# Optimization experiments

Hardware: AMD Instinct MI355X
Metric: run time of the kernel (lower is better)

The kernel has to match this reference:

```python
import jax, jax.numpy as jnp
import numpy as np

TOPK = 8
NGRAM = 3
D = 256
VOCAB = 5000


def build_scores_mask(seq_len, topk, ngram):
    # Replicates PREFIX.__init__ mask construction then the [:S*k,:S*k] slice
    # and the ~(...) inversion: True = disallowed (masked out).
    # Chunk-level: query chunk i may attend key chunks j in [i-1, i+ngram-2], j != i.
    L = seq_len
    allowed = np.zeros((L, L), dtype=bool)
    for i in range(L):
        for j in range(max(0, i - 1), min(L, i + ngram - 1)):
            if j != i:
                allowed[i, j] = True
    tok = np.kron(allowed, np.ones((topk, topk), dtype=bool))  # (L*k, L*k)
    return jnp.asarray(~tok)


def setup_inputs() -> dict:
    key = jax.random.key(0)
    k1, k2, k3, k4 = jax.random.split(key, 4)
    bsz, seq_len = 64, 128
    na_pred = jax.random.normal(k1, (bsz, seq_len, VOCAB), dtype=jnp.float32)
    emb_table = jax.random.normal(k2, (VOCAB, D), dtype=jnp.float32) * 0.02
    Wq = jax.random.normal(k3, (D, D), dtype=jnp.float32) / np.sqrt(D)
    Wk = jax.random.normal(k4, (D, D), dtype=jnp.float32) / np.sqrt(D)
    bq = jnp.zeros((D,), dtype=jnp.float32)
    bk = jnp.zeros((D,), dtype=jnp.float32)
    return {"bsz": bsz, "seq_len": seq_len, "na_pred": na_pred,
            "emb_table": emb_table, "Wq": Wq, "bq": bq, "Wk": Wk, "bk": bk}


def reference(bsz, seq_len, na_pred, emb_table, Wq, bq, Wk, bk):
    k, g = TOPK, NGRAM
    # top-k prefix candidates and their renormalized probabilities
    probs = jax.nn.softmax(na_pred, axis=-1)                 # (b, S, V)
    na_prefix_prob, na_prefix = jax.lax.top_k(probs, k)     # (b, S, k)
    na_prefix_prob = jax.nn.softmax(na_prefix_prob, axis=-1)
    # gather prefix embeddings (espnet-style sqrt(d) scale)
    prefix_emb = emb_table[na_prefix] * jnp.asarray(np.sqrt(D), na_pred.dtype)  # (b,S,k,D)
    prefix_emb = prefix_emb.reshape(bsz, seq_len * k, D)
    # ScoreAttention over gathered prefixes with ngram block mask
    q = prefix_emb @ Wq + bq
    kk = prefix_emb @ Wk + bk
    scores = jnp.einsum('bqd,bkd->bqk', q, kk) / jnp.asarray(np.sqrt(D), q.dtype)
    mask = build_scores_mask(seq_len, k, g)                  # (S*k, S*k) True=masked
    scores = jnp.where(mask[None], jnp.asarray(-1e9, scores.dtype), scores)
    attn = jax.nn.softmax(scores, axis=-1)                   # (b, S*k, S*k)
    # per-candidate score = incoming attention mass
    na_score = attn.sum(axis=1).reshape(bsz, seq_len, k)
    # elementwise mul with candidate prob, L1 normalize (F.normalize p=1 eps=1e-12)
    prefix_score = na_score * na_prefix_prob
    l1 = jnp.maximum(jnp.sum(jnp.abs(prefix_score), axis=-1, keepdims=True), 1e-12)
    prefix_score = prefix_score / l1                         # (b, S, k)
    # weighted reduce over candidates
    prefix_emb4 = prefix_emb.reshape(bsz, seq_len, k, D)
    scored_prefix = jnp.sum(prefix_emb4 * prefix_score[..., None], axis=2)  # (b, S, D)
    return scored_prefix, prefix_score, na_prefix
```

## Files before the change

kernel.cpp:

```cpp
#include <hip/hip_runtime.h>
#include <math.h>

#define TOPK 8
#define D    256
#define VOCAB 5000
#define BSZ  64
#define SEQ  128
#define ROWS (BSZ*SEQ)
#define NF4  (VOCAB/4)

#define OFF_IDX    0
#define OFF_NPP    262144
#define OFF_M      524288
#define OFF_W      787456
#define OFF_P      790528
#define OFF_NPART  5910528
#define OFF_KBV    6434816
#define OFF_WMAX   6455296
#define OFF_WSUM   6586368
#define OFF_WCNT   6717440
#define OFF_WCAND  6848512

#define OUT_SCORED 0
#define OUT_PS     2097152
#define OUT_IDX    2162688

typedef unsigned long long u64;
typedef unsigned int u32;

__device__ __forceinline__ float wave_fsum(float v) {
    #pragma unroll
    for (int st = 1; st < 64; st <<= 1) v += __shfl_xor(v, st, 64);
    return v;
}
__device__ __forceinline__ u64 wave_umax(u64 v) {
    #pragma unroll
    for (int st = 1; st < 64; st <<= 1) {
        const u64 o = __shfl_xor(v, st, 64);
        v = (o > v) ? o : v;
    }
    return v;
}
__device__ __forceinline__ u64 pack_key(float x, int idx) {
    u32 bu = __float_as_uint(x);
    u32 key = bu ^ ((u32)((int)bu >> 31) | 0x80000000u);
    return ((u64)key << 32) | (u64)(0xFFFFFFFFu ^ (u32)idx);
}

__global__ __launch_bounds__(256) void topk_pass1(
    const float* __restrict__ na_pred,
    float* __restrict__ wmaxA, float* __restrict__ wsumA,
    int*   __restrict__ wcntA, u64* __restrict__ wcandA)
{
    const int row  = blockIdx.x;
    const int wid  = threadIdx.x >> 6;
    const int lane = threadIdx.x & 63;
    const int wgid = row * 4 + wid;

    const float4* src = (const float4*)(na_pred + (long long)row * VOCAB) + wid * 320;
    const int nf4 = (wid == 3) ? 290 : 320;

    float4 rr[5];
    #pragma unroll
    for (int j = 0; j < 5; ++j) {
        const int i4 = lane + 64*j;
        rr[j] = (i4 < nf4) ? src[i4]
              : make_float4(-INFINITY, -INFINITY, -INFINITY, -INFINITY);
    }

    float lm = -INFINITY;
    #pragma unroll
    for (int j = 0; j < 5; ++j)
        lm = fmaxf(lm, fmaxf(fmaxf(rr[j].x, rr[j].y), fmaxf(rr[j].z, rr[j].w)));

    int c = 0;
    #pragma unroll
    for (int j = 0; j < 64; ++j) {
        const float o = __shfl(lm, j, 64);
        c += (o > lm || (o == lm && j < lane)) ? 1 : 0;
    }
    const u64 b0 = __ballot(c == 0);
    const u64 b7 = __ballot(c == 7);
    const float wmax = __shfl(lm, (int)(__ffsll(b0) - 1), 64);
    const float thr  = __shfl(lm, (int)(__ffsll(b7) - 1), 64);

    float se = 0.f;
    #pragma unroll
    for (int j = 0; j < 5; ++j) {
        se += __expf(rr[j].x - wmax) + __expf(rr[j].y - wmax)
            + __expf(rr[j].z - wmax) + __expf(rr[j].w - wmax);
    }
    const float S = wave_fsum(se);

    int ct = 0;
    #pragma unroll
    for (int j = 0; j < 5; ++j)
        ct += (rr[j].x >= thr) + (rr[j].y >= thr) + (rr[j].z >= thr) + (rr[j].w >= thr);

    int v = ct;
    #pragma unroll
    for (int d = 1; d < 64; d <<= 1) {
        const int o = __shfl_up(v, d, 64);
        if (lane >= d) v += o;
    }
    const int total = __shfl(v, 63, 64);

    u64* myc = wcandA + (long long)wgid * 64;
    int run = v - ct;
    #pragma unroll
    for (int j = 0; j < 5; ++j) {
        const int e0 = wid*1280 + 4*(lane + 64*j);
        const float vv[4] = {rr[j].x, rr[j].y, rr[j].z, rr[j].w};
        #pragma unroll
        for (int cc = 0; cc < 4; ++cc) {
            if (vv[cc] >= thr) {
                if (run < 64) myc[run] = pack_key(vv[cc], e0 + cc);
                ++run;
            }
        }
    }
    if (lane == 63) {
        wmaxA[wgid] = wmax;
        wsumA[wgid] = S;
        wcntA[wgid] = total;
    }
}

__global__ __launch_bounds__(256) void topk_pass2(
    const float* __restrict__ na_pred,
    const float* __restrict__ wmaxA, const float* __restrict__ wsumA,
    const int*   __restrict__ wcntA, const u64* __restrict__ wcandA,
    int*  __restrict__ out_idx,
    float* __restrict__ out_npp,
    float* __restrict__ out_idx_f)
{
    __shared__ u64   ck[256];
    __shared__ float wm4[4], ws4[4];
    __shared__ int   wc4[4];
    __shared__ u64   res_s[8];
    __shared__ u64   ured[4];

    const int row = blockIdx.x;
    const int tid = threadIdx.x;
    const int lane = tid & 63;
    const int wid  = tid >> 6;

    if (tid < 4) {
        wm4[tid] = wmaxA[row*4 + tid];
        ws4[tid] = wsumA[row*4 + tid];
        wc4[tid] = wcntA[row*4 + tid];
    }
    if (tid < 8) res_s[tid] = 0xFFFFFFFFULL;
    __syncthreads();

    const int c0 = wc4[0], c1 = wc4[1], c2 = wc4[2], c3 = wc4[3];
    const bool ovf = (c0 > 64) || (c1 > 64) || (c2 > 64) || (c3 > 64);
    const float rowmax = fmaxf(fmaxf(wm4[0], wm4[1]), fmaxf(wm4[2], wm4[3]));
    const float S = ws4[0]*__expf(wm4[0]-rowmax) + ws4[1]*__expf(wm4[1]-rowmax)
                  + ws4[2]*__expf(wm4[2]-rowmax) + ws4[3]*__expf(wm4[3]-rowmax);

    const int cw = min(wc4[wid], 64);
    u64 mine = 0ULL;
    if (lane < cw) mine = wcandA[(long long)(row*4 + wid)*64 + lane];
    ck[tid] = mine;
    __syncthreads();

    if (!ovf) {
        const int n0 = min(c0,64), n1 = min(c1,64), n2 = min(c2,64), n3 = min(c3,64);
        int c = 0;
        for (int j = 0;       j < n0;       ++j) c += (ck[j]       > mine) ? 1 : 0;
        for (int j = 0;       j < n1;       ++j) c += (ck[64+j]    > mine) ? 1 : 0;
        for (int j = 0;       j < n2;       ++j) c += (ck[128+j]   > mine) ? 1 : 0;
        for (int j = 0;       j < n3;       ++j) c += (ck[192+j]   > mine) ? 1 : 0;
        if (mine != 0ULL && c < 8) res_s[c] = mine;
    } else {
        const float4* srcr = (const float4*)(na_pred + (long long)row * VOCAB);
        const int i0 = tid, i1 = tid+256, i2 = tid+512, i3 = tid+768, i4 = tid+1024;
        const float4 r0 = srcr[i0];
        const float4 r1 = srcr[i1];
        const float4 r2 = srcr[i2];
        const float4 r3 = srcr[i3];
        const float4 r4 = (i4 < NF4) ? srcr[i4]
                        : make_float4(-INFINITY, -INFINITY, -INFINITY, -INFINITY);
        u64 last = ~0ULL;
        #pragma unroll 1
        for (int r = 0; r < 8; ++r) {
            u64 best = 0ULL;
#define CAND(val, eidx) do { const u64 k_ = pack_key((val), (eidx)); \
    if (k_ < last && k_ > best) best = k_; } while (0)
            CAND(r0.x, 4*i0+0); CAND(r0.y, 4*i0+1); CAND(r0.z, 4*i0+2); CAND(r0.w, 4*i0+3);
            CAND(r1.x, 4*i1+0); CAND(r1.y, 4*i1+1); CAND(r1.z, 4*i1+2); CAND(r1.w, 4*i1+3);
            CAND(r2.x, 4*i2+0); CAND(r2.y, 4*i2+1); CAND(r2.z, 4*i2+2); CAND(r2.w, 4*i2+3);
            CAND(r3.x, 4*i3+0); CAND(r3.y, 4*i3+1); CAND(r3.z, 4*i3+2); CAND(r3.w, 4*i3+3);
            CAND(r4.x, 4*i4+0); CAND(r4.y, 4*i4+1); CAND(r4.z, 4*i4+2); CAND(r4.w, 4*i4+3);
#undef CAND
            best = wave_umax(best);
            if (lane == 0) ured[wid] = best;
            __syncthreads();
            u64 b = ured[0];
            #pragma unroll
            for (int wq = 1; wq < 4; ++wq) b = (ured[wq] > b) ? ured[wq] : b;
            if (tid == 0) res_s[r] = b;
            last = b;
            __syncthreads();
        }
    }
    __syncthreads();

    if (wid == 0 && lane < 8) {
        const u64 res = res_s[lane];
        const u32 key = (u32)(res >> 32);
        const int ixv = (int)(0xFFFFFFFFu ^ (u32)(res & 0xFFFFFFFFu));
        const u32 bu  = key ^ ((key & 0x80000000u) ? 0x80000000u : 0xFFFFFFFFu);
        const float p = __expf(__uint_as_float(bu) - rowmax) / S;
        float pm = p;
        #pragma unroll
        for (int st = 1; st < 8; st <<= 1) pm = fmaxf(pm, __shfl_xor(pm, st, 64));
        const float q = __expf(p - pm);
        float s2 = q;
        #pragma unroll
        for (int st = 1; st < 8; st <<= 1) s2 += __shfl_xor(s2, st, 64);
        const long long ob = (long long)row * TOPK + lane;
        out_idx[ob]   = ixv;
        out_npp[ob]   = q / s2;
        out_idx_f[ob] = (float)ixv;
    }
}

__global__ __launch_bounds__(256) void mw_kernel(
    const float* __restrict__ Wq, const float* __restrict__ Wk,
    const float* __restrict__ bq,
    float* __restrict__ M, float* __restrict__ w)
{
    __shared__ float qrow[D];
    const int j = threadIdx.x;
    if (blockIdx.x < D) {
        const int a = blockIdx.x;
        qrow[j] = Wq[a*D + j];
        __syncthreads();
        float acc = 0.f;
        #pragma unroll 4
        for (int d4 = 0; d4 < 64; ++d4) {
            const float4 wk = *(const float4*)&Wk[j*D + 4*d4];
            const float4 q4 = *(const float4*)&qrow[4*d4];
            acc += wk.x*q4.x + wk.y*q4.y + wk.z*q4.z + wk.w*q4.w;
        }
        M[a*D + j] = acc;
    } else {
        float aw = 0.f;
        #pragma unroll 4
        for (int d4 = 0; d4 < 64; ++d4) {
            const float4 wk = *(const float4*)&Wk[j*D + 4*d4];
            const float4 b4 = *(const float4*)&bq[4*d4];
            aw += wk.x*b4.x + wk.y*b4.y + wk.z*b4.z + wk.w*b4.w;
        }
        w[j] = aw;
    }
}

__global__ __launch_bounds__(256) void kbv_kernel(
    const float* __restrict__ E, const float* __restrict__ w,
    float* __restrict__ kbv)
{
    const int row  = blockIdx.x * 4 + (threadIdx.x >> 6);
    const int lane = threadIdx.x & 63;
    if (row >= VOCAB) return;
    const float4 e  = *(const float4*)&E[(long long)row*D + 4*lane];
    const float4 ww = *(const float4*)&w[4*lane];
    float p = e.x*ww.x + e.y*ww.y + e.z*ww.z + e.w*ww.w;
    #pragma unroll
    for (int st = 1; st < 64; st <<= 1) p += __shfl_xor(p, st, 64);
    if (lane == 0) kbv[row] = p;
}

__global__ __launch_bounds__(256) void p_kernel(
    const float* __restrict__ E, const float* __restrict__ M,
    float* __restrict__ P)
{
    __shared__ float seT[256][20];
    const int tid = threadIdx.x;
    const int r0  = blockIdx.x * 16;
    {
        const int r = tid >> 4, d4b = tid & 15;
        const bool ok = (r0 + r) < VOCAB;
        #pragma unroll
        for (int k = 0; k < 4; ++k) {
            const int d4 = d4b + 16*k;
            float4 v = make_float4(0.f, 0.f, 0.f, 0.f);
            if (ok) v = *(const float4*)&E[(long long)(r0+r)*D + 4*d4];
            seT[4*d4+0][r] = v.x; seT[4*d4+1][r] = v.y;
            seT[4*d4+2][r] = v.z; seT[4*d4+3][r] = v.w;
        }
    }
    __syncthreads();
    const int rg = tid >> 6, j4 = tid & 63;
    float acc[4][4];
    #pragma unroll
    for (int i = 0; i < 4; ++i)
        { acc[i][0]=0.f; acc[i][1]=0.f; acc[i][2]=0.f; acc[i][3]=0.f; }
    #pragma unroll 4
    for (int d = 0; d < 256; ++d) {
        const float4 m4 = *(const float4*)&M[d*D + 4*j4];
        const float4 s4 = *(const float4*)&seT[d][4*rg];
        const float ss[4] = {s4.x, s4.y, s4.z, s4.w};
        #pragma unroll
        for (int rr = 0; rr < 4; ++rr) {
            acc[rr][0] += ss[rr]*m4.x; acc[rr][1] += ss[rr]*m4.y;
            acc[rr][2] += ss[rr]*m4.z; acc[rr][3] += ss[rr]*m4.w;
        }
    }
    #pragma unroll
    for (int rr = 0; rr < 4; ++rr) {
        const int row = r0 + 4*rg + rr;
        if (row < VOCAB) {
            float4 o;
            o.x = acc[rr][0]; o.y = acc[rr][1]; o.z = acc[rr][2]; o.w = acc[rr][3];
            *(float4*)&P[(long long)row*D + 4*j4] = o;
        }
    }
}

__global__ __launch_bounds__(64) void attn_kernel(
    const float* __restrict__ P, const float* __restrict__ E,
    const int*  __restrict__ idx, const float* __restrict__ kbv,
    float* __restrict__ na_part )
{
    const int blk = blockIdx.x;
    const int b = blk >> 7, s = blk & 127;
    const int tid = threadIdx.x;

    __shared__ float Ps[8][260];
    __shared__ float Es[16][260];
    __shared__ int   qidx[8];
    __shared__ int   kidx[16];
    __shared__ float kb[16];
    __shared__ int   kchs[2];

    int kcl[2]; int nk = 0;
    if (s > 0)       kcl[nk++] = s - 1;
    if (s < SEQ - 1) kcl[nk++] = s + 1;
    const int nkeys = nk * 8;

    if (tid < 2 && tid < nk) kchs[tid] = kcl[tid];
    if (tid < 8) qidx[tid] = idx[blk*8 + tid];
    if (tid < 16) {
        if (tid < nkeys) {
            const int v = idx[(b*SEQ + kcl[tid >> 3])*8 + (tid & 7)];
            kidx[tid] = v;
            kb[tid]   = kbv[v];
        } else { kidx[tid] = 0; kb[tid] = 0.f; }
    }
    __syncthreads();

    #pragma unroll
    for (int r = 0; r < 8; ++r)
        *(float4*)&Ps[r][4*tid] = *(const float4*)&P[(long long)qidx[r]*D + 4*tid];
    for (int r = 0; r < 16; ++r)
        if (r < nkeys)
            *(float4*)&Es[r][4*tid] = *(const float4*)&E[(long long)kidx[r]*D + 4*tid];
    __syncthreads();

    const int qp = tid >> 4, ki = tid & 15;
    float acc0 = 0.f, acc1 = 0.f;
    const float* pr0 = Ps[qp];
    const float* pr1 = Ps[qp + 4];
    const float* er  = Es[ki];
    #pragma unroll 4
    for (int d4 = 0; d4 < 64; ++d4) {
        const float4 e  = *(const float4*)&er[4*d4];
        const float4 p0 = *(const float4*)&pr0[4*d4];
        const float4 p1 = *(const float4*)&pr1[4*d4];
        acc0 += p0.x*e.x + p0.y*e.y + p0.z*e.z + p0.w*e.w;
        acc1 += p1.x*e.x + p1.y*e.y + p1.z*e.z + p1.w*e.w;
    }
    const bool kvalid = ki < nkeys;
    const float s0 = kvalid ? (16.f*acc0 + kb[ki]) : -1e30f;
    const float s1 = kvalid ? (16.f*acc1 + kb[ki]) : -1e30f;

    float m0 = s0, m1 = s1;
    #pragma unroll
    for (int st = 1; st < 16; st <<= 1) {
        m0 = fmaxf(m0, __shfl_xor(m0, st, 64));
        m1 = fmaxf(m1, __shfl_xor(m1, st, 64));
    }
    float e0 = kvalid ? __expf(s0 - m0) : 0.f;
    float e1 = kvalid ? __expf(s1 - m1) : 0.f;
    float t0 = e0, t1 = e1;
    #pragma unroll
    for (int st = 1; st < 16; st <<= 1) {
        t0 += __shfl_xor(t0, st, 64);
        t1 += __shfl_xor(t1, st, 64);
    }
    const float a0 = e0 / t0, a1 = e1 / t1;

    float cs = a0 + a1;
    cs += __shfl_xor(cs, 16, 64);
    cs += __shfl_xor(cs, 32, 64);
    if (tid < 16 && kvalid) {
        const int kc   = kchs[tid >> 3];
        const int slot = (kc == s + 1) ? 0 : 1;
        na_part[((b*SEQ + kc)*2 + slot)*8 + (tid & 7)] = cs;
    }
}

__global__ __launch_bounds__(256) void finalize_kernel(
    const float* __restrict__ E, const int* __restrict__ idx,
    const float* __restrict__ npp, const float* __restrict__ na_part,
    float* __restrict__ out)
{
    const int blk = blockIdx.x;
    const int s   = blk & 127;
    const int tid = threadIdx.x;
    __shared__ float ps[8];
    __shared__ int   id8[8];

    if (tid < 8) {
        const long long t = (long long)blk*8 + tid;
        float ns = 0.f;
        if (s >= 1)       ns += na_part[((long long)blk*2 + 0)*8 + tid];
        if (s <= SEQ - 2) ns += na_part[((long long)blk*2 + 1)*8 + tid];
        ps[tid] = ns * npp[t];
        id8[tid] = idx[t];
    }
    __syncthreads();
    if (tid == 0) {
        float l1 = 0.f;
        #pragma unroll
        for (int r = 0; r < 8; ++r) l1 += fabsf(ps[r]);
        l1 = fmaxf(l1, 1e-12f);
        #pragma unroll
        for (int r = 0; r < 8; ++r) ps[r] /= l1;
    }
    __syncthreads();

    float acc = 0.f;
    #pragma unroll
    for (int r = 0; r < 8; ++r) acc += E[(long long)id8[r]*D + tid] * ps[r];
    out[OUT_SCORED + (long long)blk*D + tid] = acc * 16.f;
    if (tid < 8) out[OUT_PS + (long long)blk*8 + tid] = ps[tid];
}

extern "C" void kernel_launch(void* const* d_in, const int* in_sizes, int n_in,
                              void* d_out, int out_size, void* d_ws, size_t ws_size,
                              hipStream_t stream)
{
    const float* na_pred = (const float*)d_in[2];
    const float* emb     = (const float*)d_in[3];
    const float* Wq      = (const float*)d_in[4];
    const float* bq      = (const float*)d_in[5];
    const float* Wk      = (const float*)d_in[6];
    const float* bk      = (const float*)d_in[7];
    (void)bk;

    char* ws = (char*)d_ws;
    int*   ws_idx  = (int*)  (ws + OFF_IDX);
    float* ws_npp  = (float*)(ws + OFF_NPP);
    float* ws_M    = (float*)(ws + OFF_M);
    float* ws_w    = (float*)(ws + OFF_W);
    float* ws_P    = (float*)(ws + OFF_P);
    float* ws_np   = (float*)(ws + OFF_NPART);
    float* ws_kbv  = (float*)(ws + OFF_KBV);
    float* ws_wmax = (float*)(ws + OFF_WMAX);
    float* ws_wsum = (float*)(ws + OFF_WSUM);
    int*   ws_wcnt = (int*)  (ws + OFF_WCNT);
    u64*   ws_wcnd = (u64*)  (ws + OFF_WCAND);
    float* out     = (float*)d_out;

    topk_pass1<<<ROWS, 256, 0, stream>>>(na_pred, ws_wmax, ws_wsum, ws_wcnt, ws_wcnd);
    topk_pass2<<<ROWS, 256, 0, stream>>>(na_pred, ws_wmax, ws_wsum, ws_wcnt, ws_wcnd,
                                         ws_idx, ws_npp, out + OUT_IDX);
    mw_kernel<<<D + 1, 256, 0, stream>>>(Wq, Wk, bq, ws_M, ws_w);
    kbv_kernel<<<(VOCAB + 3)/4, 256, 0, stream>>>(emb, ws_w, ws_kbv);
    p_kernel<<<(VOCAB + 15)/16, 256, 0, stream>>>(emb, ws_M, ws_P);
    attn_kernel<<<ROWS, 64, 0, stream>>>(ws_P, emb, ws_idx, ws_kbv, ws_np);
    finalize_kernel<<<ROWS, 256, 0, stream>>>(emb, ws_idx, ws_npp, ws_np, out);
}
```

Before: 142.0 us.

## Fuse two-pass top-k into one kernel with 4 rows per block and prefetch

Merges the two top-k kernels into one, so per-wave candidates, maxima and sums stay in shared memory instead of round-tripping through global workspace. Each block now handles four rows and prefetches the next row's logits into registers while the current row is processed. The overflow fallback reuses the register-resident data instead of re-reading the row from global memory. This removes a launch and the workspace traffic, at the cost of fewer blocks (2048), more registers and serial per-row work within a block.

```diff
diff --git a/kernel.cpp b/kernel.cpp
--- a/kernel.cpp
+++ b/kernel.cpp
@@ -16,10 +16,6 @@
 #define OFF_P      790528
 #define OFF_NPART  5910528
 #define OFF_KBV    6434816
-#define OFF_WMAX   6455296
-#define OFF_WSUM   6586368
-#define OFF_WCNT   6717440
-#define OFF_WCAND  6848512
 
 #define OUT_SCORED 0
 #define OUT_PS     2097152
@@ -47,183 +43,156 @@
     return ((u64)key << 32) | (u64)(0xFFFFFFFFu ^ (u32)idx);
 }
 
-__global__ __launch_bounds__(256) void topk_pass1(
+__global__ __launch_bounds__(256) void topk_kernel(
     const float* __restrict__ na_pred,
-    float* __restrict__ wmaxA, float* __restrict__ wsumA,
-    int*   __restrict__ wcntA, u64* __restrict__ wcandA)
-{
-    const int row  = blockIdx.x;
-    const int wid  = threadIdx.x >> 6;
-    const int lane = threadIdx.x & 63;
-    const int wgid = row * 4 + wid;
-
-    const float4* src = (const float4*)(na_pred + (long long)row * VOCAB) + wid * 320;
-    const int nf4 = (wid == 3) ? 290 : 320;
-
-    float4 rr[5];
-    #pragma unroll
-    for (int j = 0; j < 5; ++j) {
-        const int i4 = lane + 64*j;
-        rr[j] = (i4 < nf4) ? src[i4]
-              : make_float4(-INFINITY, -INFINITY, -INFINITY, -INFINITY);
-    }
-
-    float lm = -INFINITY;
-    #pragma unroll
-    for (int j = 0; j < 5; ++j)
-        lm = fmaxf(lm, fmaxf(fmaxf(rr[j].x, rr[j].y), fmaxf(rr[j].z, rr[j].w)));
-
-    int c = 0;
-    #pragma unroll
-    for (int j = 0; j < 64; ++j) {
-        const float o = __shfl(lm, j, 64);
-        c += (o > lm || (o == lm && j < lane)) ? 1 : 0;
-    }
-    const u64 b0 = __ballot(c == 0);
-    const u64 b7 = __ballot(c == 7);
-    const float wmax = __shfl(lm, (int)(__ffsll(b0) - 1), 64);
-    const float thr  = __shfl(lm, (int)(__ffsll(b7) - 1), 64);
-
-    float se = 0.f;
-    #pragma unroll
-    for (int j = 0; j < 5; ++j) {
-        se += __expf(rr[j].x - wmax) + __expf(rr[j].y - wmax)
-            + __expf(rr[j].z - wmax) + __expf(rr[j].w - wmax);
-    }
-    const float S = wave_fsum(se);
-
-    int ct = 0;
-    #pragma unroll
-    for (int j = 0; j < 5; ++j)
-        ct += (rr[j].x >= thr) + (rr[j].y >= thr) + (rr[j].z >= thr) + (rr[j].w >= thr);
-
-    int v = ct;
-    #pragma unroll
-    for (int d = 1; d < 64; d <<= 1) {
-        const int o = __shfl_up(v, d, 64);
-        if (lane >= d) v += o;
-    }
-    const int total = __shfl(v, 63, 64);
-
-    u64* myc = wcandA + (long long)wgid * 64;
-    int run = v - ct;
-    #pragma unroll
-    for (int j = 0; j < 5; ++j) {
-        const int e0 = wid*1280 + 4*(lane + 64*j);
-        const float vv[4] = {rr[j].x, rr[j].y, rr[j].z, rr[j].w};
-        #pragma unroll
-        for (int cc = 0; cc < 4; ++cc) {
-            if (vv[cc] >= thr) {
-                if (run < 64) myc[run] = pack_key(vv[cc], e0 + cc);
-                ++run;
-            }
-        }
-    }
-    if (lane == 63) {
-        wmaxA[wgid] = wmax;
-        wsumA[wgid] = S;
-        wcntA[wgid] = total;
-    }
-}
-
-__global__ __launch_bounds__(256) void topk_pass2(
-    const float* __restrict__ na_pred,
-    const float* __restrict__ wmaxA, const float* __restrict__ wsumA,
-    const int*   __restrict__ wcntA, const u64* __restrict__ wcandA,
     int*  __restrict__ out_idx,
     float* __restrict__ out_npp,
     float* __restrict__ out_idx_f)
 {
-    __shared__ u64   ck[256];
+    __shared__ u64   ck[4][64];
     __shared__ float wm4[4], ws4[4];
     __shared__ int   wc4[4];
     __shared__ u64   res_s[8];
     __shared__ u64   ured[4];
 
-    const int row = blockIdx.x;
-    const int tid = threadIdx.x;
+    const int tid  = threadIdx.x;
     const int lane = tid & 63;
     const int wid  = tid >> 6;
-
-    if (tid < 4) {
-        wm4[tid] = wmaxA[row*4 + tid];
-        ws4[tid] = wsumA[row*4 + tid];
-        wc4[tid] = wcntA[row*4 + tid];
-    }
-    if (tid < 8) res_s[tid] = 0xFFFFFFFFULL;
-    __syncthreads();
-
-    const int c0 = wc4[0], c1 = wc4[1], c2 = wc4[2], c3 = wc4[3];
-    const bool ovf = (c0 > 64) || (c1 > 64) || (c2 > 64) || (c3 > 64);
-    const float rowmax = fmaxf(fmaxf(wm4[0], wm4[1]), fmaxf(wm4[2], wm4[3]));
-    const float S = ws4[0]*__expf(wm4[0]-rowmax) + ws4[1]*__expf(wm4[1]-rowmax)
-                  + ws4[2]*__expf(wm4[2]-rowmax) + ws4[3]*__expf(wm4[3]-rowmax);
-
-    const int cw = min(wc4[wid], 64);
-    u64 mine = 0ULL;
-    if (lane < cw) mine = wcandA[(long long)(row*4 + wid)*64 + lane];
-    ck[tid] = mine;
-    __syncthreads();
-
-    if (!ovf) {
-        const int n0 = min(c0,64), n1 = min(c1,64), n2 = min(c2,64), n3 = min(c3,64);
+    const bool tail_ok = (wid < 3) || (lane < 34);
+    const float4 NEGI = make_float4(-INFINITY, -INFINITY, -INFINITY, -INFINITY);
+
+    const float4* s0 = (const float4*)(na_pred + (long long)(blockIdx.x*4) * VOCAB) + wid * 320;
+    float4 B0 = s0[lane];
+    float4 B1 = s0[lane + 64];
+    float4 B2 = s0[lane + 128];
+    float4 B3 = s0[lane + 192];
+    float4 B4 = tail_ok ? s0[lane + 256] : NEGI;
+
+    #pragma unroll 1
+    for (int rep = 0; rep < 4; ++rep) {
+        const int row = blockIdx.x*4 + rep;
+
+        const float4 A0 = B0, A1 = B1, A2 = B2, A3 = B3, A4 = B4;
+        if (rep < 3) {
+            const float4* sn = (const float4*)(na_pred + (long long)(row+1) * VOCAB) + wid * 320;
+            B0 = sn[lane];
+            B1 = sn[lane + 64];
+            B2 = sn[lane + 128];
+            B3 = sn[lane + 192];
+            B4 = tail_ok ? sn[lane + 256] : NEGI;
+        }
+
+        if (tid < 8) res_s[tid] = 0xFFFFFFFFULL;
+
+        float lm = fmaxf(fmaxf(A0.x, A0.y), fmaxf(A0.z, A0.w));
+        lm = fmaxf(lm, fmaxf(fmaxf(A1.x, A1.y), fmaxf(A1.z, A1.w)));
+        lm = fmaxf(lm, fmaxf(fmaxf(A2.x, A2.y), fmaxf(A2.z, A2.w)));
+        lm = fmaxf(lm, fmaxf(fmaxf(A3.x, A3.y), fmaxf(A3.z, A3.w)));
+        lm = fmaxf(lm, fmaxf(fmaxf(A4.x, A4.y), fmaxf(A4.z, A4.w)));
+
         int c = 0;
-        for (int j = 0;       j < n0;       ++j) c += (ck[j]       > mine) ? 1 : 0;
-        for (int j = 0;       j < n1;       ++j) c += (ck[64+j]    > mine) ? 1 : 0;
-        for (int j = 0;       j < n2;       ++j) c += (ck[128+j]   > mine) ? 1 : 0;
-        for (int j = 0;       j < n3;       ++j) c += (ck[192+j]   > mine) ? 1 : 0;
-        if (mine != 0ULL && c < 8) res_s[c] = mine;
-    } else {
-        const float4* srcr = (const float4*)(na_pred + (long long)row * VOCAB);
-        const int i0 = tid, i1 = tid+256, i2 = tid+512, i3 = tid+768, i4 = tid+1024;
-        const float4 r0 = srcr[i0];
-        const float4 r1 = srcr[i1];
-        const float4 r2 = srcr[i2];
-        const float4 r3 = srcr[i3];
-        const float4 r4 = (i4 < NF4) ? srcr[i4]
-                        : make_float4(-INFINITY, -INFINITY, -INFINITY, -INFINITY);
-        u64 last = ~0ULL;
-        #pragma unroll 1
-        for (int r = 0; r < 8; ++r) {
-            u64 best = 0ULL;
-#define CAND(val, eidx) do { const u64 k_ = pack_key((val), (eidx)); \
+        #pragma unroll
+        for (int j = 0; j < 64; ++j) {
+            const float o = __shfl(lm, j, 64);
+            c += (o > lm || (o == lm && j < lane)) ? 1 : 0;
+        }
+        const u64 b0 = __ballot(c == 0);
+        const u64 b7 = __ballot(c == 7);
+        const float wmax = __shfl(lm, (int)(__ffsll(b0) - 1), 64);
+        const float thr  = __shfl(lm, (int)(__ffsll(b7) - 1), 64);
+
+        float se = 0.f;
+        se += __expf(A0.x - wmax) + __expf(A0.y - wmax) + __expf(A0.z - wmax) + __expf(A0.w - wmax);
+        se += __expf(A1.x - wmax) + __expf(A1.y - wmax) + __expf(A1.z - wmax) + __expf(A1.w - wmax);
+        se += __expf(A2.x - wmax) + __expf(A2.y - wmax) + __expf(A2.z - wmax) + __expf(A2.w - wmax);
+        se += __expf(A3.x - wmax) + __expf(A3.y - wmax) + __expf(A3.z - wmax) + __expf(A3.w - wmax);
+        se += __expf(A4.x - wmax) + __expf(A4.y - wmax) + __expf(A4.z - wmax) + __expf(A4.w - wmax);
+        const float S = wave_fsum(se);
+
+        int ct = 0;
+        ct += (A0.x >= thr) + (A0.y >= thr) + (A0.z >= thr) + (A0.w >= thr);
+        ct += (A1.x >= thr) + (A1.y >= thr) + (A1.z >= thr) + (A1.w >= thr);
+        ct += (A2.x >= thr) + (A2.y >= thr) + (A2.z >= thr) + (A2.w >= thr);
+        ct += (A3.x >= thr) + (A3.y >= thr) + (A3.z >= thr) + (A3.w >= thr);
+        ct += (A4.x >= thr) + (A4.y >= thr) + (A4.z >= thr) + (A4.w >= thr);
+
+        int v = ct;
+        #pragma unroll
+        for (int d = 1; d < 64; d <<= 1) {
+            const int o = __shfl_up(v, d, 64);
+            if (lane >= d) v += o;
+        }
+        int run = v - ct;
+#define STORE(val, j, cc) do { const float x_ = (val); \
+        if (x_ >= thr) { if (run < 64) ck[wid][run] = pack_key(x_, wid*1280 + 4*(lane + 64*(j)) + (cc)); ++run; } } while (0)
+        STORE(A0.x,0,0); STORE(A0.y,0,1); STORE(A0.z,0,2); STORE(A0.w,0,3);
+        STORE(A1.x,1,0); STORE(A1.y,1,1); STORE(A1.z,1,2); STORE(A1.w,1,3);
+        STORE(A2.x,2,0); STORE(A2.y,2,1); STORE(A2.z,2,2); STORE(A2.w,2,3);
+        STORE(A3.x,3,0); STORE(A3.y,3,1); STORE(A3.z,3,2); STORE(A3.w,3,3);
+        STORE(A4.x,4,0); STORE(A4.y,4,1); STORE(A4.z,4,2); STORE(A4.w,4,3);
+#undef STORE
+        if (lane == 63) { wm4[wid] = wmax; ws4[wid] = S; wc4[wid] = v; }
+        __syncthreads();
+
+        const int c0 = wc4[0], c1 = wc4[1], c2 = wc4[2], c3 = wc4[3];
+        const bool ovf = (c0 > 64) || (c1 > 64) || (c2 > 64) || (c3 > 64);
+
+        if (!ovf) {
+            const u64 mine = (lane < wc4[wid]) ? ck[wid][lane] : 0ULL;
+            int r = 0;
+            for (int j = 0; j < c0; ++j) r += (ck[0][j] > mine) ? 1 : 0;
+            for (int j = 0; j < c1; ++j) r += (ck[1][j] > mine) ? 1 : 0;
+            for (int j = 0; j < c2; ++j) r += (ck[2][j] > mine) ? 1 : 0;
+            for (int j = 0; j < c3; ++j) r += (ck[3][j] > mine) ? 1 : 0;
+            if (mine != 0ULL && r < 8) res_s[r] = mine;
+        } else {
+            u64 last = ~0ULL;
+            #pragma unroll 1
+            for (int r = 0; r < 8; ++r) {
+                u64 best = 0ULL;
+#define CAND(val, j, cc) do { const u64 k_ = pack_key((val), wid*1280 + 4*(lane + 64*(j)) + (cc)); \
     if (k_ < last && k_ > best) best = k_; } while (0)
-            CAND(r0.x, 4*i0+0); CAND(r0.y, 4*i0+1); CAND(r0.z, 4*i0+2); CAND(r0.w, 4*i0+3);
-            CAND(r1.x, 4*i1+0); CAND(r1.y, 4*i1+1); CAND(r1.z, 4*i1+2); CAND(r1.w, 4*i1+3);
-            CAND(r2.x, 4*i2+0); CAND(r2.y, 4*i2+1); CAND(r2.z, 4*i2+2); CAND(r2.w, 4*i2+3);
-            CAND(r3.x, 4*i3+0); CAND(r3.y, 4*i3+1); CAND(r3.z, 4*i3+2); CAND(r3.w, 4*i3+3);
-            CAND(r4.x, 4*i4+0); CAND(r4.y, 4*i4+1); CAND(r4.z, 4*i4+2); CAND(r4.w, 4*i4+3);
+                CAND(A0.x,0,0); CAND(A0.y,0,1); CAND(A0.z,0,2); CAND(A0.w,0,3);
+                CAND(A1.x,1,0); CAND(A1.y,1,1); CAND(A1.z,1,2); CAND(A1.w,1,3);
+                CAND(A2.x,2,0); CAND(A2.y,2,1); CAND(A2.z,2,2); CAND(A2.w,2,3);
+                CAND(A3.x,3,0); CAND(A3.y,3,1); CAND(A3.z,3,2); CAND(A3.w,3,3);
+                CAND(A4.x,4,0); CAND(A4.y,4,1); CAND(A4.z,4,2); CAND(A4.w,4,3);
 #undef CAND
-            best = wave_umax(best);
-            if (lane == 0) ured[wid] = best;
-            __syncthreads();
-            u64 b = ured[0];
+                best = wave_umax(best);
+                if (lane == 0) ured[wid] = best;
+                __syncthreads();
+                u64 b = ured[0];
+                #pragma unroll
+                for (int wq = 1; wq < 4; ++wq) b = (ured[wq] > b) ? ured[wq] : b;
+                if (tid == 0) res_s[r] = b;
+                last = b;
+                __syncthreads();
+            }
+        }
+        __syncthreads();
+
+        if (tid < 8) {
+            const float rowmax = fmaxf(fmaxf(wm4[0], wm4[1]), fmaxf(wm4[2], wm4[3]));
+            const float St = ws4[0]*__expf(wm4[0]-rowmax) + ws4[1]*__expf(wm4[1]-rowmax)
+                           + ws4[2]*__expf(wm4[2]-rowmax) + ws4[3]*__expf(wm4[3]-rowmax);
+            const u64 res = res_s[tid];
+            const u32 key = (u32)(res >> 32);
+            const int ixv = (int)(0xFFFFFFFFu ^ (u32)(res & 0xFFFFFFFFu));
+            const u32 bu  = key ^ ((key & 0x80000000u) ? 0x80000000u : 0xFFFFFFFFu);
+            const float p = __expf(__uint_as_float(bu) - rowmax) / St;
+            float pm = p;
             #pragma unroll
-            for (int wq = 1; wq < 4; ++wq) b = (ured[wq] > b) ? ured[wq] : b;
-            if (tid == 0) res_s[r] = b;
-            last = b;
-            __syncthreads();
-        }
-    }
-    __syncthreads();
-
-    if (wid == 0 && lane < 8) {
-        const u64 res = res_s[lane];
-        const u32 key = (u32)(res >> 32);
-        const int ixv = (int)(0xFFFFFFFFu ^ (u32)(res & 0xFFFFFFFFu));
-        const u32 bu  = key ^ ((key & 0x80000000u) ? 0x80000000u : 0xFFFFFFFFu);
-        const float p = __expf(__uint_as_float(bu) - rowmax) / S;
-        float pm = p;
-        #pragma unroll
-        for (int st = 1; st < 8; st <<= 1) pm = fmaxf(pm, __shfl_xor(pm, st, 64));
-        const float q = __expf(p - pm);
-        float s2 = q;
-        #pragma unroll
-        for (int st = 1; st < 8; st <<= 1) s2 += __shfl_xor(s2, st, 64);
-        const long long ob = (long long)row * TOPK + lane;
-        out_idx[ob]   = ixv;
-        out_npp[ob]   = q / s2;
-        out_idx_f[ob] = (float)ixv;
+            for (int st = 1; st < 8; st <<= 1) pm = fmaxf(pm, __shfl_xor(pm, st, 64));
+            const float q = __expf(p - pm);
+            float s2 = q;
+            #pragma unroll
+            for (int st = 1; st < 8; st <<= 1) s2 += __shfl_xor(s2, st, 64);
+            const long long ob = (long long)row * TOPK + tid;
+            out_idx[ob]   = ixv;
+            out_npp[ob]   = q / s2;
+            out_idx_f[ob] = (float)ixv;
+        }
+        __syncthreads();
     }
 }
 
@@ -460,15 +429,9 @@
     float* ws_P    = (float*)(ws + OFF_P);
     float* ws_np   = (float*)(ws + OFF_NPART);
     float* ws_kbv  = (float*)(ws + OFF_KBV);
-    float* ws_wmax = (float*)(ws + OFF_WMAX);
-    float* ws_wsum = (float*)(ws + OFF_WSUM);
-    int*   ws_wcnt = (int*)  (ws + OFF_WCNT);
-    u64*   ws_wcnd = (u64*)  (ws + OFF_WCAND);
     float* out     = (float*)d_out;
 
-    topk_pass1<<<ROWS, 256, 0, stream>>>(na_pred, ws_wmax, ws_wsum, ws_wcnt, ws_wcnd);
-    topk_pass2<<<ROWS, 256, 0, stream>>>(na_pred, ws_wmax, ws_wsum, ws_wcnt, ws_wcnd,
-                                         ws_idx, ws_npp, out + OUT_IDX);
+    topk_kernel<<<ROWS/4, 256, 0, stream>>>(na_pred, ws_idx, ws_npp, out + OUT_IDX);
     mw_kernel<<<D + 1, 256, 0, stream>>>(Wq, Wk, bq, ws_M, ws_w);
     kbv_kernel<<<(VOCAB + 3)/4, 256, 0, stream>>>(emb, ws_w, ws_kbv);
     p_kernel<<<(VOCAB + 15)/16, 256, 0, stream>>>(emb, ws_M, ws_P);
```

New measurement: 185.6 us. 1.31x slower.
